# Performance work log

Hardware: AMD Instinct MI355X
Metric: run time of the kernel (lower is better)

## Reference

```python
import jax, jax.numpy as jnp
import numpy as np

B, S, D, H = 2, 1024, 512, 8  # batch, seq, per-head dim (=in_dim), n_heads
NEG_INF = -1e30  # matches torch -inf after exp underflow, grad-safe


def _linear_init(key, fan_in, fan_out, bias=True):
    kw, kb = jax.random.split(key)
    bound = 1.0 / np.sqrt(fan_in)
    W = jax.random.uniform(kw, (fan_in, fan_out), jnp.float32, -bound, bound)
    if not bias:
        return W
    b = jax.random.uniform(kb, (fan_out,), jnp.float32, -bound, bound)
    return W, b


def setup_inputs() -> dict:
    key = jax.random.key(0)
    ks = jax.random.split(key, 8)
    x = jax.random.normal(ks[0], (B, S, D), jnp.float32)
    y = jax.random.normal(ks[1], (B, S, D), jnp.float32)
    Wq, bq = _linear_init(ks[2], D, H * D)          # query: Linear(in_dim, out_dim*H)
    Wk, bk = _linear_init(ks[3], D, H * D)          # key
    Wv, bv = _linear_init(ks[4], D, H * D)          # value
    Wp = _linear_init(ks[5], D, D, bias=False)      # projection: Linear(y_in_dim, y_out_dim//H, bias=False)
    gamma = jax.random.uniform(ks[6], (H, 1, 1, 1), jnp.float32) + 0.001
    mask = jax.random.bernoulli(ks[7], 0.95, (S,))  # True = keep column
    return dict(x=x, y=y, Wq=Wq, bq=bq, Wk=Wk, bk=bk, Wv=Wv, bv=bv, Wp=Wp,
                gamma=gamma, mask=mask)


def reference(x, y, Wq, bq, Wk, bk, Wv, bv, Wp, gamma, mask):
    b, s, _ = x.shape
    h = gamma.shape[0]
    # projections, then head-major split (split_cat along feature dim -> batch dim)
    q = (x @ Wq + bq).reshape(b, s, h, -1).transpose(2, 0, 1, 3)  # (h,B,S,d)
    k = (y @ Wk + bk).reshape(b, s, h, -1).transpose(2, 0, 1, 3)  # (h,B,S,d)
    v = (y @ Wv + bv).reshape(b, s, h, -1).transpose(2, 0, 1, 3)  # (h,B,S,dv)
    # energy = bmm(q, k^T)  (no scaling in the original)
    energy = jnp.einsum('hbsd,hbtd->hbst', q, k)                  # (h,B,S,S)
    # boolean column mask: energy[..., ~mask] = -inf
    energy = jnp.where(mask[None, None, None, :], energy, NEG_INF)
    attn = jax.nn.softmax(energy, axis=-1)
    # out = bmm(attention^T, v): out[t] = sum_s attn[s, t] * v[s]
    out = jnp.einsum('hbst,hbsv->hbtv', attn, v)                  # (h,B,S,dv)
    # gamma-weighted residual blend against projected x (broadcast over heads)
    xp = x @ Wp                                                   # (B,S,dv)
    out = (gamma * out + xp[None]) / (gamma + 1.0)                # (h,B,S,dv)
    return out.transpose(1, 0, 2, 3)                              # (B,h,S,dv)
```

## Files before the change

kernel.cpp:

```cpp
#include <hip/hip_runtime.h>
#include <stdint.h>

#define Bb 2
#define Ss 1024
#define Dd 512
#define Hh 8
#define HD 4096
#define Mm 2048

typedef _Float16 f16x8 __attribute__((ext_vector_type(8)));
typedef _Float16 f16x4 __attribute__((ext_vector_type(4)));
typedef float    f32x4 __attribute__((ext_vector_type(4)));

#define LOG2E 1.44269504f

#define GLOAD16(g, l)                                                          \
    __builtin_amdgcn_global_load_lds(                                          \
        (const __attribute__((address_space(1))) void*)(g),                    \
        (__attribute__((address_space(3))) void*)(l), 16, 0, 0)

__global__ __launch_bounds__(256) void cvt_f16(
    const float* __restrict__ in, _Float16* __restrict__ out, int n)
{
    int i = (blockIdx.x * 256 + threadIdx.x) * 4;
    if (i < n) {
        float4 u = *(const float4*)(in + i);
        f16x4 o;
        o[0] = (_Float16)u.x; o[1] = (_Float16)u.y;
        o[2] = (_Float16)u.z; o[3] = (_Float16)u.w;
        *(f16x4*)(out + i) = o;
    }
}

__global__ __launch_bounds__(256) void cvt_w_pk(
    const float* __restrict__ W, int ld, int col0,
    _Float16* __restrict__ out, int NC)
{
    const int n  = blockIdx.x * 256 + threadIdx.x;
    const int k0 = blockIdx.y * 8;
    f16x8 o;
#pragma unroll
    for (int j = 0; j < 8; j++)
        o[j] = (_Float16)W[(size_t)(k0 + j) * ld + col0 + n];
    *(f16x8*)(out + ((size_t)(k0 >> 3) * NC + n) * 8) = o;
}

__global__ __launch_bounds__(256) void stage_all(
    const float* __restrict__ x, const float* __restrict__ y,
    const float* __restrict__ Wq, const float* __restrict__ Wk,
    const float* __restrict__ Wv, const float* __restrict__ Wp,
    _Float16* __restrict__ xf, _Float16* __restrict__ yf,
    _Float16* __restrict__ Wbuf, int NCq, size_t wslot)
{
    const int f = blockIdx.x;
    if (f < 2048) {
        const float* in = (f < 1024) ? x : y;
        _Float16* out   = (f < 1024) ? xf : yf;
        const int i = ((f & 1023) * 256 + threadIdx.x) * 4;
        float4 u = *(const float4*)(in + i);
        f16x4 o;
        o[0] = (_Float16)u.x; o[1] = (_Float16)u.y;
        o[2] = (_Float16)u.z; o[3] = (_Float16)u.w;
        *(f16x4*)(out + i) = o;
        return;
    }
    int l = f - 2048;
    const float* W; int ld, NCz, z, bx, by;
    if (l < 3072) {
        z = l >> 10; l &= 1023;
        W = (z == 0) ? Wq : (z == 1) ? Wk : Wv; ld = HD; NCz = NCq;
        bx = l & 15; by = l >> 4;
    } else {
        z = 3; l -= 3072;
        W = Wp; ld = Dd; NCz = Dd;
        bx = l & 1; by = l >> 1;
    }
    const int n  = bx * 256 + threadIdx.x;
    const int k0 = by * 8;
    f16x8 o;
#pragma unroll
    for (int j = 0; j < 8; j++)
        o[j] = (_Float16)W[(size_t)(k0 + j) * ld + n];
    *(f16x8*)(Wbuf + (size_t)z * wslot + ((size_t)(k0 >> 3) * NCz + n) * 8) = o;
}

__device__ __forceinline__ void proj_body(
    const _Float16* __restrict__ A, const _Float16* __restrict__ Wpk,
    const float* __restrict__ bias, int bias0,
    _Float16* __restrict__ C, int NC, int packC, int bx, int by)
{
    __shared__ _Float16 lsA[2][4096];
    __shared__ _Float16 lsB[2][4096];
    const int t = threadIdx.x;
    const int lane = t & 63, wave = t >> 6;
    const int quad = lane >> 4, l15 = lane & 15;
    const int m0b = by * 128, n0b = bx * 128;
    const int aw = (wave >> 1) * 64, bw = (wave & 1) * 64;
    const int qx = (quad ^ ((l15 >> 2) & 3)) * 8;

    const _Float16* ag = A + (size_t)(m0b + (t >> 2)) * Dd
                           + ((t & 3) ^ ((t >> 4) & 3)) * 8;
    const _Float16* bg = Wpk + ((size_t)(t >> 7) * NC + n0b + (t & 127)) * 8;
    const size_t arj = (size_t)64 * Dd;
    const size_t bcs = (size_t)NC * 8;

    f32x4 acc[4][4] = {};
    GLOAD16(ag,           &lsA[0][t * 8]);
    GLOAD16(ag + arj,     &lsA[0][t * 8 + 2048]);
    GLOAD16(bg,           &lsB[0][t * 8]);
    GLOAD16(bg + 2 * bcs, &lsB[0][t * 8 + 2048]);
    __syncthreads();
    int cur = 0;
    for (int kb = 0; kb < Dd; kb += 32) {
        if (kb + 32 < Dd) {
            const int nb = cur ^ 1;
            GLOAD16(ag + kb + 32,       &lsA[nb][t * 8]);
            GLOAD16(ag + arj + kb + 32, &lsA[nb][t * 8 + 2048]);
            GLOAD16(bg + (size_t)((kb >> 3) + 4) * bcs, &lsB[nb][t * 8]);
            GLOAD16(bg + (size_t)((kb >> 3) + 6) * bcs, &lsB[nb][t * 8 + 2048]);
        }
        f16x8 af[4], bf[4];
#pragma unroll
        for (int mi = 0; mi < 4; mi++)
            af[mi] = *(const f16x8*)&lsA[cur][(aw + mi * 16 + l15) * 32 + qx];
#pragma unroll
        for (int ni = 0; ni < 4; ni++)
            bf[ni] = *(const f16x8*)&lsB[cur][quad * 1024 + (bw + ni * 16 + l15) * 8];
#pragma unroll
        for (int mi = 0; mi < 4; mi++)
#pragma unroll
            for (int ni = 0; ni < 4; ni++)
                acc[mi][ni] = __builtin_amdgcn_mfma_f32_16x16x32_f16(af[mi], bf[ni], acc[mi][ni], 0, 0, 0);
        __syncthreads();
        cur ^= 1;
    }

#pragma unroll
    for (int mi = 0; mi < 4; mi++) {
        const int row0 = m0b + aw + mi * 16 + quad * 4;
#pragma unroll
        for (int ni = 0; ni < 4; ni++) {
            const int col = n0b + bw + ni * 16 + l15;
            const float bv = bias ? bias[bias0 + col] : 0.0f;
            if (packC) {
                f16x4 o;
#pragma unroll
                for (int r = 0; r < 4; r++) o[r] = (_Float16)(acc[mi][ni][r] + bv);
                *(f16x4*)(C + ((size_t)(row0 >> 3) * NC + col) * 8 + (row0 & 7)) = o;
            } else {
#pragma unroll
                for (int r = 0; r < 4; r++)
                    C[(size_t)(row0 + r) * NC + col] = (_Float16)(acc[mi][ni][r] + bv);
            }
        }
    }
}

__global__ __launch_bounds__(256, 4) void proj_f16(
    const _Float16* __restrict__ A, const _Float16* __restrict__ Wpk,
    const float* __restrict__ bias, int bias0,
    _Float16* __restrict__ C, int NC, int packC)
{
    proj_body(A, Wpk, bias, bias0, C, NC, packC, blockIdx.x, blockIdx.y);
}

__global__ __launch_bounds__(256, 4) void proj_flat(
    const _Float16* __restrict__ xf, const _Float16* __restrict__ yf,
    const _Float16* __restrict__ Wpk, size_t wslot,
    const float* __restrict__ bq, const float* __restrict__ bk,
    const float* __restrict__ bv,
    _Float16* __restrict__ qb, _Float16* __restrict__ kb,
    _Float16* __restrict__ vb, _Float16* __restrict__ xp)
{
    const int f = blockIdx.x;
    int z, bx, by;
    if (f < 1536) { z = f >> 9; const int r = f & 511; bx = r & 31; by = r >> 5; }
    else         { z = 3;      const int r = f - 1536; bx = r & 3;  by = r >> 2; }
    const _Float16* A = (z == 0 || z == 3) ? xf : yf;
    const _Float16* W = Wpk + (size_t)z * wslot;
    const float* bias = (z == 0) ? bq : (z == 1) ? bk : (z == 2) ? bv : nullptr;
    _Float16* C = (z == 0) ? qb : (z == 1) ? kb : (z == 2) ? vb : xp;
    const int NCz = (z == 3) ? Dd : (Hh * Dd);
    proj_body(A, W, bias, 0, C, NCz, z == 2, bx, by);
}

__global__ __launch_bounds__(256, 4) void energy_f16(
    const _Float16* __restrict__ Q, const _Float16* __restrict__ Kb,
    const int* __restrict__ mask, _Float16* __restrict__ E,
    float* __restrict__ part, int NC)
{
    __shared__ _Float16 lsA[2][4096];
    __shared__ _Float16 lsB[2][4096];
    const int zl = blockIdx.x;
    const int b = zl & 1, hloc = zl >> 1;
    const _Float16* qz = Q + (size_t)b * Ss * NC + hloc * Dd;
    const _Float16* kz = Kb + (size_t)b * Ss * NC + hloc * Dd;
    _Float16* Ez = E + (size_t)zl * Ss * Ss;

    const int t = threadIdx.x;
    const int lane = t & 63, wave = t >> 6;
    const int quad = lane >> 4, l15 = lane & 15;
    const int sb = blockIdx.y * 128;
    const int tb = blockIdx.z * 128;
    const int sw = (wave >> 1) * 64, tw = (wave & 1) * 64;
    const int qx = (quad ^ ((l15 >> 2) & 3)) * 8;

    const int sc = ((t & 3) ^ ((t >> 4) & 3)) * 8;
    const _Float16* ag = qz + (size_t)(sb + (t >> 2)) * NC + sc;
    const _Float16* bg = kz + (size_t)(tb + (t >> 2)) * NC + sc;
    const size_t rj = (size_t)64 * NC;

    f32x4 acc[4][4] = {};
    GLOAD16(ag,      &lsA[0][t * 8]);
    GLOAD16(ag + rj, &lsA[0][t * 8 + 2048]);
    GLOAD16(bg,      &lsB[0][t * 8]);
    GLOAD16(bg + rj, &lsB[0][t * 8 + 2048]);
    __syncthreads();
    int cur = 0;
    for (int kb = 0; kb < Dd; kb += 32) {
        if (kb + 32 < Dd) {
            const int nb = cur ^ 1;
            GLOAD16(ag + kb + 32,      &lsA[nb][t * 8]);
            GLOAD16(ag + rj + kb + 32, &lsA[nb][t * 8 + 2048]);
            GLOAD16(bg + kb + 32,      &lsB[nb][t * 8]);
            GLOAD16(bg + rj + kb + 32, &lsB[nb][t * 8 + 2048]);
        }
        f16x8 af[4], bf[4];
#pragma unroll
        for (int mi = 0; mi < 4; mi++)
            af[mi] = *(const f16x8*)&lsA[cur][(sw + mi * 16 + l15) * 32 + qx];
#pragma unroll
        for (int ni = 0; ni < 4; ni++)
            bf[ni] = *(const f16x8*)&lsB[cur][(tw + ni * 16 + l15) * 32 + qx];
#pragma unroll
        for (int mi = 0; mi < 4; mi++)
#pragma unroll
            for (int ni = 0; ni < 4; ni++)
                acc[mi][ni] = __builtin_amdgcn_mfma_f32_16x16x32_f16(af[mi], bf[ni], acc[mi][ni], 0, 0, 0);
        __syncthreads();
        cur ^= 1;
    }

#pragma unroll
    for (int ni = 0; ni < 4; ni++) {
        const int tcol = tb + tw + ni * 16 + l15;
        const int keep = mask[tcol];
#pragma unroll
        for (int mi = 0; mi < 4; mi++)
#pragma unroll
            for (int r = 0; r < 4; r++)
                acc[mi][ni][r] = keep ? acc[mi][ni][r] : -30000.0f;
    }

#pragma unroll
    for (int mi = 0; mi < 4; mi++) {
        const int s0 = sb + sw + mi * 16 + quad * 4;
        _Float16* base = Ez + (size_t)(s0 >> 3) * (Ss * 8) + (s0 & 7);
#pragma unroll
        for (int ni = 0; ni < 4; ni++) {
            const int tcol = tb + tw + ni * 16 + l15;
            f16x4 o;
#pragma unroll
            for (int r = 0; r < 4; r++) {
                o[r] = (_Float16)acc[mi][ni][r];
                acc[mi][ni][r] = (float)o[r];
            }
            *(f16x4*)(base + (size_t)tcol * 8) = o;
        }
    }

    const int jc = blockIdx.z * 2 + (wave & 1);
    float* ps = part + ((size_t)(zl * 16 + jc) * 1024) * 2;
#pragma unroll
    for (int mi = 0; mi < 4; mi++) {
#pragma unroll
        for (int r = 0; r < 4; r++) {
            float m = fmaxf(fmaxf(acc[mi][0][r], acc[mi][1][r]),
                            fmaxf(acc[mi][2][r], acc[mi][3][r]));
#pragma unroll
            for (int off = 1; off < 16; off <<= 1) m = fmaxf(m, __shfl_xor(m, off));
            float l = __expf(acc[mi][0][r] - m) + __expf(acc[mi][1][r] - m)
                    + __expf(acc[mi][2][r] - m) + __expf(acc[mi][3][r] - m);
#pragma unroll
            for (int off = 1; off < 16; off <<= 1) l += __shfl_xor(l, off);
            if (l15 == 0) {
                const int s = sb + sw + mi * 16 + quad * 4 + r;
                ps[s * 2]     = m;
                ps[s * 2 + 1] = l;
            }
        }
    }
}

__global__ __launch_bounds__(256, 4) void pv_f16(
    const _Float16* __restrict__ Epk, const _Float16* __restrict__ Vpk,
    const _Float16* __restrict__ Xp, const float* __restrict__ G,
    const float* __restrict__ part, float* __restrict__ Out, int h0, int NC)
{
    __shared__ _Float16 lsP[2][2048];
    __shared__ _Float16 lsV[2][4096];
    __shared__ float lsC[1024];
    const int zl = blockIdx.x;
    const int b = zl & 1, hloc = zl >> 1;
    const int h = h0 + hloc;
    const _Float16* az = Epk + (size_t)zl * Ss * Ss;

    const int t = threadIdx.x;
    const int lane = t & 63, wave = t >> 6;
    const int quad = lane >> 4, l15 = lane & 15;
    const int tb = blockIdx.y * 64;
    const int cb = blockIdx.z * 128;
    const int tw = (wave >> 1) * 32, cw = (wave & 1) * 64;

    const _Float16* pg = az + ((size_t)(t >> 6) * Ss + tb + (t & 63)) * 8;
    const _Float16* vg = Vpk + (((size_t)((b * Ss) >> 3) + (t >> 7)) * NC
                                + hloc * Dd + cb + (t & 127)) * 8;
    const size_t acs = (size_t)Ss * 8;
    const size_t vcs = (size_t)NC * 8;

    f32x4 acc[2][4] = {};
    GLOAD16(pg,           &lsP[0][t * 8]);
    GLOAD16(vg,           &lsV[0][t * 8]);
    GLOAD16(vg + 2 * vcs, &lsV[0][t * 8 + 2048]);
    {
        const float* pz = part + (size_t)zl * 16 * 1024 * 2;
        for (int ss = t; ss < 1024; ss += 256) {
            const float* p = pz + (size_t)ss * 2;
            float m = -3.4e38f;
#pragma unroll
            for (int j = 0; j < 16; j++) m = fmaxf(m, p[(size_t)j * 2048]);
            float l = 0.0f;
#pragma unroll
            for (int j = 0; j < 16; j++)
                l += p[(size_t)j * 2048 + 1] * __expf(p[(size_t)j * 2048] - m);
            lsC[ss] = -(m + __logf(l)) * LOG2E;
        }
    }
    __syncthreads();
    int cur = 0;
    for (int kb = 0; kb < Ss; kb += 32) {
        if (kb + 32 < Ss) {
            const int nb = cur ^ 1;
            GLOAD16(pg + ((size_t)(kb >> 3) + 4) * acs, &lsP[nb][t * 8]);
            GLOAD16(vg + ((size_t)(kb >> 3) + 4) * vcs, &lsV[nb][t * 8]);
            GLOAD16(vg + ((size_t)(kb >> 3) + 6) * vcs, &lsV[nb][t * 8 + 2048]);
        }
        const float4 c0 = *(const float4*)&lsC[kb + quad * 8];
        const float4 c1 = *(const float4*)&lsC[kb + quad * 8 + 4];
        const float nc[8] = {c0.x, c0.y, c0.z, c0.w, c1.x, c1.y, c1.z, c1.w};
        f16x8 af[2], bf[4];
#pragma unroll
        for (int mi = 0; mi < 2; mi++) {
            const f16x8 raw = *(const f16x8*)&lsP[cur][quad * 512 + (tw + mi * 16 + l15) * 8];
#pragma unroll
            for (int j = 0; j < 8; j++)
                af[mi][j] = (_Float16)__builtin_amdgcn_exp2f(
                                fmaf((float)raw[j], LOG2E, nc[j]));
        }
#pragma unroll
        for (int ni = 0; ni < 4; ni++)
            bf[ni] = *(const f16x8*)&lsV[cur][quad * 1024 + (cw + ni * 16 + l15) * 8];
#pragma unroll
        for (int mi = 0; mi < 2; mi++)
#pragma unroll
            for (int ni = 0; ni < 4; ni++)
                acc[mi][ni] = __builtin_amdgcn_mfma_f32_16x16x32_f16(af[mi], bf[ni], acc[mi][ni], 0, 0, 0);
        __syncthreads();
        cur ^= 1;
    }

    const float g = G[h];
    const float inv = 1.0f / (g + 1.0f);
#pragma unroll
    for (int mi = 0; mi < 2; mi++) {
        const int tr0 = tb + tw + mi * 16 + quad * 4;
#pragma unroll
        for (int r = 0; r < 4; r++) {
            const int tt = tr0 + r;
            const _Float16* xrow = Xp + (size_t)(b * Ss + tt) * Dd;
            float* orow = Out + ((size_t)((b * Hh + h) * Ss + tt)) * Dd;
#pragma unroll
            for (int ni = 0; ni < 4; ni++) {
                const int c = cb + cw + ni * 16 + l15;
                orow[c] = (g * acc[mi][ni][r] + (float)xrow[c]) * inv;
            }
        }
    }
}

extern "C" void kernel_launch(void* const* d_in, const int* in_sizes, int n_in,
                              void* d_out, int out_size, void* d_ws, size_t ws_size,
                              hipStream_t stream) {
    const float* x    = (const float*)d_in[0];
    const float* y    = (const float*)d_in[1];
    const float* Wq   = (const float*)d_in[2];
    const float* bq   = (const float*)d_in[3];
    const float* Wk   = (const float*)d_in[4];
    const float* bk   = (const float*)d_in[5];
    const float* Wv   = (const float*)d_in[6];
    const float* bv   = (const float*)d_in[7];
    const float* Wp   = (const float*)d_in[8];
    const float* gm   = (const float*)d_in[9];
    const int*   mask = (const int*)d_in[10];

    const int HG = (ws_size >= (size_t)134217728) ? 8 : 4;
    const int NC = HG * Dd;
    const int NZ = 2 * HG;
    const size_t wslot = (size_t)512 * NC;

    char* ws = (char*)d_ws;
    size_t off = 0;
    _Float16* Wbuf = (_Float16*)(ws + off); off += (size_t)(HG == 8 ? 4 : 1) * wslot * 2;
    _Float16* qb   = (_Float16*)(ws + off); off += (size_t)Mm * NC * 2;
    _Float16* kb   = (_Float16*)(ws + off); off += (size_t)Mm * NC * 2;
    _Float16* vb   = (_Float16*)(ws + off); off += (size_t)Mm * NC * 2;
    _Float16* xp   = (_Float16*)(ws + off); off += (size_t)Mm * Dd * 2;
    _Float16* en   = (_Float16*)(ws + off); off += (size_t)NZ * Ss * Ss * 2;
    float*    part = (float*)(ws + off);    off += (size_t)NZ * 16 * 1024 * 2 * 4;
    _Float16* xf   = en;
    _Float16* yf   = en + (size_t)Mm * 512;

    dim3 blk(256);
    const int NXY = Mm * 512;

    if (HG == 8) {
        stage_all<<<dim3(5248), blk, 0, stream>>>(x, y, Wq, Wk, Wv, Wp,
                                                  xf, yf, Wbuf, NC, wslot);
        proj_flat<<<dim3(1600), blk, 0, stream>>>(xf, yf, Wbuf, wslot,
                                                  bq, bk, bv, qb, kb, vb, xp);
        energy_f16<<<dim3(NZ, 8, 8), blk, 0, stream>>>(qb, kb, mask, en, part, NC);
        pv_f16<<<dim3(NZ, 16, 4), blk, 0, stream>>>(en, vb, xp, gm, part,
                                                    (float*)d_out, 0, NC);
    } else {
        cvt_f16<<<dim3(NXY / 1024), blk, 0, stream>>>(x, xf, NXY);
        cvt_w_pk<<<dim3(2, 64), blk, 0, stream>>>(Wp, Dd, 0, Wbuf, Dd);
        proj_f16<<<dim3(4, 16), blk, 0, stream>>>(xf, Wbuf, nullptr, 0, xp, Dd, 0);

        for (int h0 = 0; h0 < Hh; h0 += HG) {
            cvt_f16<<<dim3(NXY / 1024), blk, 0, stream>>>(x, xf, NXY);
            cvt_f16<<<dim3(NXY / 1024), blk, 0, stream>>>(y, yf, NXY);

            cvt_w_pk<<<dim3(NC / 256, 64), blk, 0, stream>>>(Wq, HD, h0 * Dd, Wbuf, NC);
            proj_f16<<<dim3(NC / 128, 16), blk, 0, stream>>>(xf, Wbuf, bq, h0 * Dd, qb, NC, 0);
            cvt_w_pk<<<dim3(NC / 256, 64), blk, 0, stream>>>(Wk, HD, h0 * Dd, Wbuf, NC);
            proj_f16<<<dim3(NC / 128, 16), blk, 0, stream>>>(yf, Wbuf, bk, h0 * Dd, kb, NC, 0);
            cvt_w_pk<<<dim3(NC / 256, 64), blk, 0, stream>>>(Wv, HD, h0 * Dd, Wbuf, NC);
            proj_f16<<<dim3(NC / 128, 16), blk, 0, stream>>>(yf, Wbuf, bv, h0 * Dd, vb, NC, 1);

            energy_f16<<<dim3(NZ, 8, 8), blk, 0, stream>>>(qb, kb, mask, en, part, NC);
            pv_f16<<<dim3(NZ, 16, 4), blk, 0, stream>>>(en, vb, xp, gm, part,
                                                        (float*)d_out, h0, NC);
        }
    }
}
```

Measured before the change: 215.7 us.

## Store unnormalized exp scores in QK kernel and rescale with per-row fp16 factor

The QK kernel now writes exp(e - local_max) as fp16 probabilities instead of raw logits, reusing the exp values it already computes for the partial row sums. The PV kernel replaces its per-element exp2 with a single fp16 packed multiply by a per-row scale exp(m_local - logsumexp), computed once per block from the chunk matching blockIdx.y. This moves the transcendental work out of the PV inner loop. It relies on the QK column-chunk index matching the PV t-block index, and an fp16 scale factor may underflow for rows whose local max is far below the global one.

```diff
diff --git a/kernel.cpp b/kernel.cpp
--- a/kernel.cpp
+++ b/kernel.cpp
@@ -248,45 +248,49 @@
 #pragma unroll
         for (int mi = 0; mi < 4; mi++)
 #pragma unroll
-            for (int r = 0; r < 4; r++)
-                acc[mi][ni][r] = keep ? acc[mi][ni][r] : -30000.0f;
-    }
-
+            for (int r = 0; r < 4; r++) {
+                const float v = keep ? acc[mi][ni][r] : -30000.0f;
+                acc[mi][ni][r] = (float)(_Float16)v;
+            }
+    }
+
+    const int jc = blockIdx.z * 2 + (wave & 1);
+    float* ps = part + ((size_t)(zl * 16 + jc) * 1024) * 2;
 #pragma unroll
     for (int mi = 0; mi < 4; mi++) {
         const int s0 = sb + sw + mi * 16 + quad * 4;
         _Float16* base = Ez + (size_t)(s0 >> 3) * (Ss * 8) + (s0 & 7);
+        float m[4], l[4];
+#pragma unroll
+        for (int r = 0; r < 4; r++) {
+            float mm = fmaxf(fmaxf(acc[mi][0][r], acc[mi][1][r]),
+                             fmaxf(acc[mi][2][r], acc[mi][3][r]));
+#pragma unroll
+            for (int off = 1; off < 16; off <<= 1) mm = fmaxf(mm, __shfl_xor(mm, off));
+            m[r] = mm;
+            l[r] = 0.0f;
+        }
 #pragma unroll
         for (int ni = 0; ni < 4; ni++) {
             const int tcol = tb + tw + ni * 16 + l15;
             f16x4 o;
 #pragma unroll
             for (int r = 0; r < 4; r++) {
-                o[r] = (_Float16)acc[mi][ni][r];
-                acc[mi][ni][r] = (float)o[r];
+                const float p = __expf(acc[mi][ni][r] - m[r]);
+                l[r] += p;
+                o[r] = (_Float16)p;
             }
             *(f16x4*)(base + (size_t)tcol * 8) = o;
         }
-    }
-
-    const int jc = blockIdx.z * 2 + (wave & 1);
-    float* ps = part + ((size_t)(zl * 16 + jc) * 1024) * 2;
-#pragma unroll
-    for (int mi = 0; mi < 4; mi++) {
 #pragma unroll
         for (int r = 0; r < 4; r++) {
-            float m = fmaxf(fmaxf(acc[mi][0][r], acc[mi][1][r]),
-                            fmaxf(acc[mi][2][r], acc[mi][3][r]));
-#pragma unroll
-            for (int off = 1; off < 16; off <<= 1) m = fmaxf(m, __shfl_xor(m, off));
-            float l = __expf(acc[mi][0][r] - m) + __expf(acc[mi][1][r] - m)
-                    + __expf(acc[mi][2][r] - m) + __expf(acc[mi][3][r] - m);
-#pragma unroll
-            for (int off = 1; off < 16; off <<= 1) l += __shfl_xor(l, off);
+            float ll = l[r];
+#pragma unroll
+            for (int off = 1; off < 16; off <<= 1) ll += __shfl_xor(ll, off);
             if (l15 == 0) {
-                const int s = sb + sw + mi * 16 + quad * 4 + r;
-                ps[s * 2]     = m;
-                ps[s * 2 + 1] = l;
+                const int s = s0 + r;
+                ps[s * 2]     = m[r];
+                ps[s * 2 + 1] = ll;
             }
         }
     }
@@ -299,7 +303,7 @@
 {
     __shared__ _Float16 lsP[2][2048];
     __shared__ _Float16 lsV[2][4096];
-    __shared__ float lsC[1024];
+    __shared__ _Float16 lsS[1024];
     const int zl = blockIdx.x;
     const int b = zl & 1, hloc = zl >> 1;
     const int h = h0 + hloc;
@@ -311,6 +315,7 @@
     const int tb = blockIdx.y * 64;
     const int cb = blockIdx.z * 128;
     const int tw = (wave >> 1) * 32, cw = (wave & 1) * 64;
+    const int jc0 = blockIdx.y;
 
     const _Float16* pg = az + ((size_t)(t >> 6) * Ss + tb + (t & 63)) * 8;
     const _Float16* vg = Vpk + (((size_t)((b * Ss) >> 3) + (t >> 7)) * NC
@@ -333,7 +338,8 @@
 #pragma unroll
             for (int j = 0; j < 16; j++)
                 l += p[(size_t)j * 2048 + 1] * __expf(p[(size_t)j * 2048] - m);
-            lsC[ss] = -(m + __logf(l)) * LOG2E;
+            const float C = m + __logf(l);
+            lsS[ss] = (_Float16)__expf(p[(size_t)jc0 * 2048] - C);
         }
     }
     __syncthreads();
@@ -345,17 +351,12 @@
             GLOAD16(vg + ((size_t)(kb >> 3) + 4) * vcs, &lsV[nb][t * 8]);
             GLOAD16(vg + ((size_t)(kb >> 3) + 6) * vcs, &lsV[nb][t * 8 + 2048]);
         }
-        const float4 c0 = *(const float4*)&lsC[kb + quad * 8];
-        const float4 c1 = *(const float4*)&lsC[kb + quad * 8 + 4];
-        const float nc[8] = {c0.x, c0.y, c0.z, c0.w, c1.x, c1.y, c1.z, c1.w};
+        const f16x8 sc8 = *(const f16x8*)&lsS[kb + quad * 8];
         f16x8 af[2], bf[4];
 #pragma unroll
         for (int mi = 0; mi < 2; mi++) {
-            const f16x8 raw = *(const f16x8*)&lsP[cur][quad * 512 + (tw + mi * 16 + l15) * 8];
-#pragma unroll
-            for (int j = 0; j < 8; j++)
-                af[mi][j] = (_Float16)__builtin_amdgcn_exp2f(
-                                fmaf((float)raw[j], LOG2E, nc[j]));
+            const f16x8 pu = *(const f16x8*)&lsP[cur][quad * 512 + (tw + mi * 16 + l15) * 8];
+            af[mi] = pu * sc8;
         }
 #pragma unroll
         for (int ni = 0; ni < 4; ni++)
```

After: 205.2 us, median of 2. -4.9%, faster.
